# Kernel tuning notes

Hardware: AMD Instinct MI355X
Metric: run time of the kernel (lower is better)

## Reference

```python
import jax, jax.numpy as jnp
import numpy as np

H, KV, D = 16, 4, 128
EPS = 1e-6

def setup_inputs() -> dict:
    key = jax.random.key(0)
    ks = jax.random.split(key, 7)
    B, S, HS = 2, 2048, 2048
    return {
        "hidden_states": jax.random.normal(ks[0], (B, S, HS), jnp.float32),
        "cos": jax.random.uniform(ks[1], (S, D), jnp.float32),
        "sin": jax.random.uniform(ks[2], (S, D), jnp.float32),
        "Wq": jax.random.normal(ks[3], (H * D, HS), jnp.float32) * 0.02,
        "Wk": jax.random.normal(ks[4], (KV * D, HS), jnp.float32) * 0.02,
        "Wv": jax.random.normal(ks[5], (KV * D, HS), jnp.float32) * 0.02,
        "Wo": jax.random.normal(ks[6], (HS, H * D), jnp.float32) * 0.02,
        "norm_q_w": jnp.ones((D,), jnp.float32),
        "norm_k_w": jnp.ones((D,), jnp.float32),
    }

def _rmsnorm(x, w):
    # RMSNorm over head_dim
    return x * jax.lax.rsqrt(jnp.mean(x * x, axis=-1, keepdims=True) + EPS) * w

def _rope(x, cos, sin):
    # x: [B, S, heads, D]; cos/sin: [S, D]; rotate-half (use_real_unbind_dim=-2)
    c = cos[None, :, None, :]
    s = sin[None, :, None, :]
    x1, x2 = jnp.split(x, 2, axis=-1)
    x_rot = jnp.concatenate([-x2, x1], axis=-1)
    return x * c + x_rot * s

def reference(hidden_states, cos, sin, Wq, Wk, Wv, Wo, norm_q_w, norm_k_w):
    B, S, _ = hidden_states.shape
    q = (hidden_states @ Wq.T).reshape(B, S, H, D)
    k = (hidden_states @ Wk.T).reshape(B, S, KV, D)
    v = (hidden_states @ Wv.T).reshape(B, S, KV, D)
    q = _rmsnorm(q, norm_q_w)
    k = _rmsnorm(k, norm_k_w)
    q = _rope(q, cos, sin)
    k = _rope(k, cos, sin)
    # GQA: repeat_interleave K/V heads to match Q heads
    g = H // KV
    k = jnp.repeat(k, g, axis=2)  # [B, S, H, D]
    v = jnp.repeat(v, g, axis=2)
    scores = jnp.einsum('bqhd,bkhd->bhqk', q, k) * (D ** -0.5)
    attn = jax.nn.softmax(scores, axis=-1)
    out = jnp.einsum('bhqk,bkhd->bqhd', attn, v)  # [B, S, H, D]
    out = out.reshape(B, S, H * D)
    return out @ Wo.T
```

## Files before the change

kernel.cpp:

```cpp
#include <hip/hip_runtime.h>


typedef __attribute__((ext_vector_type(8))) short bf16x8;
typedef __attribute__((ext_vector_type(4))) float f32x4;
typedef __attribute__((ext_vector_type(16))) float f32x16;

__device__ __forceinline__ unsigned short f2bf(float x) {
  union { float f; unsigned u; } v; v.f = x;
  unsigned r = v.u + 0x7fffu + ((v.u >> 16) & 1u);
  return (unsigned short)(r >> 16);
}

__device__ __forceinline__ float bf2f(unsigned short h) {
  union { unsigned u; float f; } v; v.u = (unsigned)h << 16;
  return v.f;
}

__device__ __forceinline__ unsigned cvt_pk_bf16(float lo, float hi) {
  unsigned r;
  asm("v_cvt_pk_bf16_f32 %0, %1, %2" : "=v"(r) : "v"(lo), "v"(hi));
  return r;
}

__device__ __forceinline__ void gload_lds16(const void* g, void* l) {
  __builtin_amdgcn_global_load_lds(
      (const __attribute__((address_space(1))) void*)g,
      (__attribute__((address_space(3))) void*)l, 16, 0, 0);
}

__global__ __launch_bounds__(256) void cvt4(const float4* __restrict__ in,
                                            ushort4* __restrict__ out, int n4) {
  int i = blockIdx.x * 256 + threadIdx.x;
  if (i < n4) {
    float4 v = in[i];
    out[i] = make_ushort4(f2bf(v.x), f2bf(v.y), f2bf(v.z), f2bf(v.w));
  }
}

template <int NF, bool OUT_BF16>
__global__ __launch_bounds__(512, 2) void gemm_bt_8ph(
    const unsigned short* __restrict__ A, const unsigned short* __restrict__ Bm,
    void* __restrict__ Cout, int M, int N, int K) {
  __shared__ char lsA[2][32768];
  __shared__ char lsB[2][NF * 8192];
  const int tid = threadIdx.x;
  const int wave = tid >> 6, lane = tid & 63;
  const int lrow = lane & 15, kg = lane >> 4;
  const int wm = wave >> 2, wn = wave & 3;
  const int BN = NF * 64;
  const int nbn = N / BN;
  const int bid = (blockIdx.x & 7) * (gridDim.x >> 3) + (blockIdx.x >> 3);
  const int m0 = (bid / nbn) << 8;
  const int n0 = (bid % nbn) * BN;
  const int NT = K >> 6;

  const int srow = tid >> 2;
  const int scol = (((tid & 3) ^ (srow & 3)) << 3);
  const size_t a0 = (size_t)(m0 + srow) * K + scol;
  const size_t a1 = (size_t)(m0 + 128 + srow) * K + scol;
  const size_t b0 = (size_t)(n0 + srow) * K + scol;
  const size_t b1 = (size_t)(n0 + 128 + srow) * K + scol;

  f32x4 acc[8][NF];
#pragma unroll
  for (int i = 0; i < 8; ++i)
#pragma unroll
    for (int j = 0; j < NF; ++j)
#pragma unroll
      for (int t = 0; t < 4; ++t) acc[i][j][t] = 0.f;

  const int xk = ((kg ^ (lrow & 3)) << 4);
  const int abase = (wm * 128 + lrow) * 64 + xk;
  const int bbase = (wn * NF * 16 + lrow) * 64 + xk;

  auto stage_plane = [&](int T, int ks) {
    if (T >= NT) return;
    const int buf = T & 1;
    const size_t kof = (size_t)T * 64 + ks * 32;
    char* da = lsA[buf] + ks * 16384 + wave * 1024;
    gload_lds16(A + a0 + kof, da);
    gload_lds16(A + a1 + kof, da + 8192);
    char* db = lsB[buf] + ks * (NF * 4096) + wave * 1024;
    gload_lds16(Bm + b0 + kof, db);
    if (NF >= 3) {
      if (tid < 256) gload_lds16(Bm + b1 + kof, db + 8192);
    }
  };

  auto phase = [&](int T, int ks, int sT, int sKs) {
    const int buf = T & 1;
    const char* pa = lsA[buf] + ks * 16384;
    const char* pb = lsB[buf] + ks * (NF * 4096);
    bf16x8 af[8], bfr[NF];
#pragma unroll
    for (int mf = 0; mf < 8; ++mf)
      af[mf] = *(const bf16x8*)(pa + abase + mf * 1024);
#pragma unroll
    for (int nf = 0; nf < NF; ++nf)
      bfr[nf] = *(const bf16x8*)(pb + bbase + nf * 1024);
    stage_plane(sT, sKs);
    asm volatile("s_waitcnt vmcnt(6)" ::: "memory");
    __builtin_amdgcn_s_barrier();
    asm volatile("s_waitcnt lgkmcnt(0)" ::: "memory");
    __builtin_amdgcn_sched_barrier(0);
    __builtin_amdgcn_s_setprio(1);
#pragma unroll
    for (int mf = 0; mf < 8; ++mf)
#pragma unroll
      for (int nf = 0; nf < NF; ++nf)
        acc[mf][nf] =
            __builtin_amdgcn_mfma_f32_16x16x32_bf16(af[mf], bfr[nf], acc[mf][nf], 0, 0, 0);
    __builtin_amdgcn_s_setprio(0);
    __builtin_amdgcn_s_barrier();
  };

  stage_plane(0, 0);
  stage_plane(0, 1);
  stage_plane(1, 0);
  asm volatile("s_waitcnt vmcnt(6)" ::: "memory");
  __builtin_amdgcn_s_barrier();

  for (int kt = 0; kt < NT; ++kt) {
    phase(kt, 0, kt + 1, 1);
    phase(kt, 1, kt + 2, 0);
  }

#pragma unroll
  for (int mf = 0; mf < 8; ++mf) {
#pragma unroll
    for (int nf = 0; nf < NF; ++nf) {
      int row = m0 + wm * 128 + mf * 16 + kg * 4;
      int col = n0 + wn * NF * 16 + nf * 16 + lrow;
      if (OUT_BF16) {
        unsigned short* C = (unsigned short*)Cout;
#pragma unroll
        for (int t = 0; t < 4; ++t)
          C[(size_t)(row + t) * N + col] = f2bf(acc[mf][nf][t]);
      } else {
        float* C = (float*)Cout;
#pragma unroll
        for (int t = 0; t < 4; ++t)
          C[(size_t)(row + t) * N + col] = acc[mf][nf][t];
      }
    }
  }
}

__global__ __launch_bounds__(256) void rms_rope(
    const unsigned short* __restrict__ QKV, const float* __restrict__ cosT,
    const float* __restrict__ sinT, const float* __restrict__ wq,
    const float* __restrict__ wk, unsigned short* __restrict__ Q,
    unsigned short* __restrict__ Kg, unsigned short* __restrict__ Vg) {
  int task = blockIdx.x * 4 + (threadIdx.x >> 6);
  int lane = threadIdx.x & 63;
  int row = task / 24;
  int slot = task - row * 24;
  int b = row >> 11, s = row & 2047;
  const unsigned short* x = QKV + (size_t)row * 3072 + slot * 128;
  float x1 = bf2f(x[lane]), x2 = bf2f(x[lane + 64]);
  if (slot < 20) {
    float ss = x1 * x1 + x2 * x2;
#pragma unroll
    for (int msk = 1; msk < 64; msk <<= 1) ss += __shfl_xor(ss, msk);
    float inv = rsqrtf(ss * (1.0f / 128.0f) + 1e-6f);
    const float* w = (slot < 16) ? wq : wk;
    x1 *= inv * w[lane];
    x2 *= inv * w[lane + 64];
    float c1 = cosT[s * 128 + lane], c2 = cosT[s * 128 + lane + 64];
    float sn1 = sinT[s * 128 + lane], sn2 = sinT[s * 128 + lane + 64];
    float o1 = x1 * c1 - x2 * sn1;
    float o2 = x2 * c2 + x1 * sn2;
    if (slot < 16) {
      const float qs = 0.08838834764831845f * 1.4426950408889634f;
      o1 *= qs; o2 *= qs;
    }
    x1 = o1; x2 = o2;
  }
  if (slot < 16) {
    unsigned short* dst = Q + (((size_t)b * 16 + slot) * 2048 + s) * 128;
    dst[lane] = f2bf(x1);
    dst[lane + 64] = f2bf(x2);
  } else {
    int kv = (slot - 16) & 3;
    size_t tb = ((size_t)((b * 4 + kv) * 32) + (s >> 6)) * 16384;
    int key = s & 63;
    if (slot < 20) {
      char* base = (char*)Kg + tb;
      int xr = (key & 7) << 4;
      *(unsigned short*)(base + key * 256 + ((lane * 2) ^ xr)) = f2bf(x1);
      *(unsigned short*)(base + key * 256 + (((lane + 64) * 2) ^ xr)) = f2bf(x2);
    } else {
      char* base = (char*)Vg + tb;
      int p = key >> 4;
      int vhi = (key >> 2) & 1;
      int e = (key & 3) | (((key >> 3) & 1) << 2);
      int off = p * 4096 + vhi * 512 + e * 2;
      int d1 = lane, d2 = lane + 64;
      *(unsigned short*)(base + off + (d1 >> 5) * 1024 + (d1 & 31) * 16) = f2bf(x1);
      *(unsigned short*)(base + off + (d2 >> 5) * 1024 + (d2 & 31) * 16) = f2bf(x2);
    }
  }
}

__global__ __launch_bounds__(256, 2) void attn64(
    const unsigned short* __restrict__ Q, const unsigned short* __restrict__ Kg,
    const unsigned short* __restrict__ Vg, unsigned short* __restrict__ O) {
  __shared__ unsigned short Kl[2][8192];
  __shared__ unsigned short Vl[2][8192];
  const int tid = threadIdx.x;
  const int wave = tid >> 6, lane = tid & 63;
  const int l31 = lane & 31, hi = lane >> 5;
  int bid = blockIdx.x;
  bid = (bid & 7) * 64 + (bid >> 3);
  const int bh = bid >> 4, qt = bid & 15;
  const int b = bh >> 4, h = bh & 15, kh = h >> 2;
  const char* Kt = (const char*)Kg + (size_t)(b * 4 + kh) * 524288;
  const char* Vt = (const char*)Vg + (size_t)(b * 4 + kh) * 524288;
  const unsigned short* Qb =
      Q + ((size_t)(b * 16 + h) * 2048 + qt * 128 + wave * 32) * 128;
  bf16x8 qf[8];
#pragma unroll
  for (int s = 0; s < 8; ++s)
    qf[s] = *(const bf16x8*)(Qb + l31 * 128 + s * 16 + hi * 8);
  f32x16 acc[4];
#pragma unroll
  for (int c = 0; c < 4; ++c)
#pragma unroll
    for (int r = 0; r < 16; ++r) acc[c][r] = 0.f;
  float lsum = 0.f;
  const int xrk = (l31 & 7) << 4;

  auto stage = [&](int t) {
    const char* kt = Kt + (size_t)t * 16384;
    const char* vt = Vt + (size_t)t * 16384;
    char* kd = (char*)Kl[t & 1];
    char* vd = (char*)Vl[t & 1];
#pragma unroll
    for (int c = 0; c < 4; ++c) {
      gload_lds16(kt + c * 4096 + tid * 16, kd + c * 4096 + wave * 1024);
      gload_lds16(vt + c * 4096 + tid * 16, vd + c * 4096 + wave * 1024);
    }
  };

  auto qk = [&](int t, f32x16& s0, f32x16& s1) {
    const char* Kb = (const char*)Kl[t & 1];
#pragma unroll
    for (int r = 0; r < 16; ++r) { s0[r] = 0.f; s1[r] = 0.f; }
#pragma unroll
    for (int s = 0; s < 8; ++s) {
      int xo = (s * 32 + hi * 16) ^ xrk;
      bf16x8 k0 = *(const bf16x8*)(Kb + l31 * 256 + xo);
      bf16x8 k1 = *(const bf16x8*)(Kb + (32 + l31) * 256 + xo);
      s0 = __builtin_amdgcn_mfma_f32_32x32x16_bf16(k0, qf[s], s0, 0, 0, 0);
      s1 = __builtin_amdgcn_mfma_f32_32x32x16_bf16(k1, qf[s], s1, 0, 0, 0);
    }
  };

  auto body = [&](int t, f32x16& c0, f32x16& c1, f32x16& n0_, f32x16& n1_) {
    float p0[16], p1[16];
#pragma unroll
    for (int r = 0; r < 16; ++r) {
      p0[r] = exp2f(c0[r]);
      p1[r] = exp2f(c1[r]);
    }
    float u8[8];
#pragma unroll
    for (int r = 0; r < 8; ++r) u8[r] = (p0[r] + p0[r + 8]) + (p1[r] + p1[r + 8]);
#pragma unroll
    for (int r = 0; r < 4; ++r) u8[r] += u8[r + 4];
    lsum += (u8[0] + u8[1]) + (u8[2] + u8[3]);
    union { bf16x8 v[4]; unsigned w[16]; } pa;
#pragma unroll
    for (int r = 0; r < 4; ++r) {
      pa.w[r]      = cvt_pk_bf16(p0[2 * r], p0[2 * r + 1]);
      pa.w[4 + r]  = cvt_pk_bf16(p0[8 + 2 * r], p0[9 + 2 * r]);
      pa.w[8 + r]  = cvt_pk_bf16(p1[2 * r], p1[2 * r + 1]);
      pa.w[12 + r] = cvt_pk_bf16(p1[8 + 2 * r], p1[9 + 2 * r]);
    }
    __syncthreads();
    __builtin_amdgcn_s_setprio(1);
    if (t + 1 < 32) qk(t + 1, n0_, n1_);
    const char* Vb = (const char*)Vl[t & 1];
#pragma unroll
    for (int p = 0; p < 4; ++p)
#pragma unroll
      for (int c = 0; c < 4; ++c) {
        bf16x8 vf = *(const bf16x8*)(Vb + p * 4096 + c * 1024 + hi * 512 + l31 * 16);
        acc[c] = __builtin_amdgcn_mfma_f32_32x32x16_bf16(pa.v[p], vf, acc[c], 0, 0, 0);
      }
    __builtin_amdgcn_s_setprio(0);
    __syncthreads();
    if (t + 2 < 32) stage(t + 2);
  };

  stage(0);
  __syncthreads();
  f32x16 s0A, s1A, s0B, s1B;
  qk(0, s0A, s1A);
  stage(1);

  for (int t = 0; t < 32; t += 2) {
    body(t, s0A, s1A, s0B, s1B);
    body(t + 1, s0B, s1B, s0A, s1A);
  }

  lsum += __shfl_xor(lsum, 32);
  float inv = 1.0f / lsum;
#pragma unroll
  for (int r = 0; r < 16; ++r) {
    int q = (r & 3) + 8 * (r >> 2) + 4 * hi;
    float invq = __shfl(inv, q);
    int srow = qt * 128 + wave * 32 + q;
    unsigned short* dst = O + (((size_t)b * 2048 + srow) * 16 + h) * 128;
#pragma unroll
    for (int c = 0; c < 4; ++c)
      dst[c * 32 + l31] = f2bf(acc[c][r] * invq);
  }
}

extern "C" void kernel_launch(void* const* d_in, const int* in_sizes, int n_in,
                              void* d_out, int out_size, void* d_ws, size_t ws_size,
                              hipStream_t stream) {
  const float* hs   = (const float*)d_in[0];
  const float* cosT = (const float*)d_in[1];
  const float* sinT = (const float*)d_in[2];
  const float* Wq   = (const float*)d_in[3];
  const float* Wk   = (const float*)d_in[4];
  const float* Wv   = (const float*)d_in[5];
  const float* Wo   = (const float*)d_in[6];
  const float* nqw  = (const float*)d_in[7];
  const float* nkw  = (const float*)d_in[8];
  float* out = (float*)d_out;

  char* ws = (char*)d_ws;
  unsigned short* X    = (unsigned short*)ws;
  unsigned short* Wqkv = X + 8388608;
  unsigned short* WoB  = Wqkv + 6291456;
  unsigned short* QKVb = WoB + 4194304;
  unsigned short* Qb   = QKVb + 12582912;
  unsigned short* Kg   = Qb + 8388608;
  unsigned short* Vg   = Kg + 2097152;
  unsigned short* Ob   = QKVb;

  cvt4<<<8192, 256, 0, stream>>>((const float4*)hs, (ushort4*)X, 2097152);
  cvt4<<<4096, 256, 0, stream>>>((const float4*)Wq, (ushort4*)Wqkv, 1048576);
  cvt4<<<1024, 256, 0, stream>>>((const float4*)Wk, (ushort4*)(Wqkv + 4194304), 262144);
  cvt4<<<1024, 256, 0, stream>>>((const float4*)Wv, (ushort4*)(Wqkv + 5242880), 262144);
  cvt4<<<4096, 256, 0, stream>>>((const float4*)Wo, (ushort4*)WoB, 1048576);

  gemm_bt_8ph<3, true><<<256, 512, 0, stream>>>(X, Wqkv, QKVb, 4096, 3072, 2048);

  rms_rope<<<24576, 256, 0, stream>>>(QKVb, cosT, sinT, nqw, nkw, Qb, Kg, Vg);

  attn64<<<512, 256, 0, stream>>>(Qb, Kg, Vg, Ob);

  gemm_bt_8ph<2, false><<<256, 512, 0, stream>>>(Ob, WoB, out, 4096, 2048, 2048);
}
```

Measured before the change: 225.7 us.

## Load V directly to registers and relayout K for conflict-free LDS reads

V tiles are now read from global memory straight into registers (16 bf16x8 per lane) instead of being staged through LDS, which halves LDS usage. K is written by the prep kernel in a new MFMA-friendly layout so LDS reads become simple strided loads with no XOR swizzle. The pipeline changes from a two-deep software-pipelined QK/PV schedule with double __syncthreads to a single barrier per tile with manual vmcnt waits. This raises register pressure and exposes global latency for V, and it loses the overlap of the next QK with the current PV.

```diff
diff --git a/kernel.cpp b/kernel.cpp
--- a/kernel.cpp
+++ b/kernel.cpp
@@ -186,9 +186,10 @@
     int key = s & 63;
     if (slot < 20) {
       char* base = (char*)Kg + tb;
-      int xr = (key & 7) << 4;
-      *(unsigned short*)(base + key * 256 + ((lane * 2) ^ xr)) = f2bf(x1);
-      *(unsigned short*)(base + key * 256 + (((lane + 64) * 2) ^ xr)) = f2bf(x2);
+      int kb = (key >> 5) * 512 + (key & 31) * 16;
+      int d1 = lane, d2 = lane + 64;
+      *(unsigned short*)(base + (d1 >> 4) * 2048 + ((d1 >> 3) & 1) * 1024 + kb + (d1 & 7) * 2) = f2bf(x1);
+      *(unsigned short*)(base + (d2 >> 4) * 2048 + ((d2 >> 3) & 1) * 1024 + kb + (d2 & 7) * 2) = f2bf(x2);
     } else {
       char* base = (char*)Vg + tb;
       int p = key >> 4;
@@ -206,7 +207,6 @@
     const unsigned short* __restrict__ Q, const unsigned short* __restrict__ Kg,
     const unsigned short* __restrict__ Vg, unsigned short* __restrict__ O) {
   __shared__ unsigned short Kl[2][8192];
-  __shared__ unsigned short Vl[2][8192];
   const int tid = threadIdx.x;
   const int wave = tid >> 6, lane = tid & 63;
   const int l31 = lane & 31, hi = lane >> 5;
@@ -228,40 +228,53 @@
 #pragma unroll
     for (int r = 0; r < 16; ++r) acc[c][r] = 0.f;
   float lsum = 0.f;
-  const int xrk = (l31 & 7) << 4;
-
-  auto stage = [&](int t) {
+
+  const char* Vlane = Vt + hi * 512 + l31 * 16;
+  bf16x8 vr[16];
+
+  auto stageK = [&](int t) {
     const char* kt = Kt + (size_t)t * 16384;
-    const char* vt = Vt + (size_t)t * 16384;
     char* kd = (char*)Kl[t & 1];
-    char* vd = (char*)Vl[t & 1];
-#pragma unroll
-    for (int c = 0; c < 4; ++c) {
+#pragma unroll
+    for (int c = 0; c < 4; ++c)
       gload_lds16(kt + c * 4096 + tid * 16, kd + c * 4096 + wave * 1024);
-      gload_lds16(vt + c * 4096 + tid * 16, vd + c * 4096 + wave * 1024);
-    }
   };
-
-  auto qk = [&](int t, f32x16& s0, f32x16& s1) {
-    const char* Kb = (const char*)Kl[t & 1];
-#pragma unroll
-    for (int r = 0; r < 16; ++r) { s0[r] = 0.f; s1[r] = 0.f; }
-#pragma unroll
-    for (int s = 0; s < 8; ++s) {
-      int xo = (s * 32 + hi * 16) ^ xrk;
-      bf16x8 k0 = *(const bf16x8*)(Kb + l31 * 256 + xo);
-      bf16x8 k1 = *(const bf16x8*)(Kb + (32 + l31) * 256 + xo);
-      s0 = __builtin_amdgcn_mfma_f32_32x32x16_bf16(k0, qf[s], s0, 0, 0, 0);
-      s1 = __builtin_amdgcn_mfma_f32_32x32x16_bf16(k1, qf[s], s1, 0, 0, 0);
-    }
+  auto loadV = [&](int t) {
+    const char* vt = Vlane + (size_t)t * 16384;
+#pragma unroll
+    for (int p = 0; p < 4; ++p)
+#pragma unroll
+      for (int c = 0; c < 4; ++c)
+        vr[p * 4 + c] = *(const bf16x8*)(vt + p * 4096 + c * 1024);
   };
 
-  auto body = [&](int t, f32x16& c0, f32x16& c1, f32x16& n0_, f32x16& n1_) {
+  loadV(0);
+  stageK(0);
+  asm volatile("s_waitcnt vmcnt(0)" ::: "memory");
+  __builtin_amdgcn_s_barrier();
+
+  f32x16 s0, s1;
+  for (int t = 0; t < 32; ++t) {
+    if (t < 31) stageK(t + 1);
+    {
+      const char* Kb = (const char*)Kl[t & 1] + hi * 1024 + l31 * 16;
+#pragma unroll
+      for (int r = 0; r < 16; ++r) { s0[r] = 0.f; s1[r] = 0.f; }
+      __builtin_amdgcn_s_setprio(1);
+#pragma unroll
+      for (int s = 0; s < 8; ++s) {
+        bf16x8 k0 = *(const bf16x8*)(Kb + s * 2048);
+        bf16x8 k1 = *(const bf16x8*)(Kb + s * 2048 + 512);
+        s0 = __builtin_amdgcn_mfma_f32_32x32x16_bf16(k0, qf[s], s0, 0, 0, 0);
+        s1 = __builtin_amdgcn_mfma_f32_32x32x16_bf16(k1, qf[s], s1, 0, 0, 0);
+      }
+      __builtin_amdgcn_s_setprio(0);
+    }
     float p0[16], p1[16];
 #pragma unroll
     for (int r = 0; r < 16; ++r) {
-      p0[r] = exp2f(c0[r]);
-      p1[r] = exp2f(c1[r]);
+      p0[r] = exp2f(s0[r]);
+      p1[r] = exp2f(s1[r]);
     }
     float u8[8];
 #pragma unroll
@@ -277,31 +290,18 @@
       pa.w[8 + r]  = cvt_pk_bf16(p1[2 * r], p1[2 * r + 1]);
       pa.w[12 + r] = cvt_pk_bf16(p1[8 + 2 * r], p1[9 + 2 * r]);
     }
-    __syncthreads();
     __builtin_amdgcn_s_setprio(1);
-    if (t + 1 < 32) qk(t + 1, n0_, n1_);
-    const char* Vb = (const char*)Vl[t & 1];
 #pragma unroll
     for (int p = 0; p < 4; ++p)
 #pragma unroll
-      for (int c = 0; c < 4; ++c) {
-        bf16x8 vf = *(const bf16x8*)(Vb + p * 4096 + c * 1024 + hi * 512 + l31 * 16);
-        acc[c] = __builtin_amdgcn_mfma_f32_32x32x16_bf16(pa.v[p], vf, acc[c], 0, 0, 0);
-      }
+      for (int c = 0; c < 4; ++c)
+        acc[c] = __builtin_amdgcn_mfma_f32_32x32x16_bf16(pa.v[p], vr[p * 4 + c], acc[c], 0, 0, 0);
     __builtin_amdgcn_s_setprio(0);
-    __syncthreads();
-    if (t + 2 < 32) stage(t + 2);
-  };
-
-  stage(0);
-  __syncthreads();
-  f32x16 s0A, s1A, s0B, s1B;
-  qk(0, s0A, s1A);
-  stage(1);
-
-  for (int t = 0; t < 32; t += 2) {
-    body(t, s0A, s1A, s0B, s1B);
-    body(t + 1, s0B, s1B, s0A, s1A);
+    if (t < 31) {
+      loadV(t + 1);
+      asm volatile("s_waitcnt vmcnt(16)" ::: "memory");
+      __builtin_amdgcn_s_barrier();
+    }
   }
 
   lsum += __shfl_xor(lsum, 32);
```

Measured after the change: 235.6 us. 1.04x slower.
